# Optimization experiments

Hardware: AMD Instinct MI355X
Metric: run time of the kernel (lower is better)

The kernel has to match this reference:

```python
import jax, jax.numpy as jnp
import numpy as np

V, D, K, O, H = 20000, 256, 16, 128, 4
NEG_INF = -1e9


def setup_inputs() -> dict:
    key = jax.random.key(0)
    k1, k2, k3, k4 = jax.random.split(key, 4)
    x = jax.random.normal(k1, (V, D), dtype=jnp.float32)
    # padded adjacency list; value V (== mask_index) marks padding slots
    adj_lst = jax.random.randint(k2, (V, K), 0, V + 1, dtype=jnp.int64)
    W = jax.random.normal(k3, (H, D, O), dtype=jnp.float32) * 0.05  # per-head linear
    a = jax.random.normal(k4, (H, O), dtype=jnp.float32) * 0.05     # per-head attn vec
    b = jnp.zeros((H, O), dtype=jnp.float32)                         # per-head bias
    return {"x": x, "W": W, "a": a, "b": b, "adj_lst": adj_lst, "mask_index": V}


def reference(x, W, a, b, adj_lst, mask_index):
    # per-head linear transform: [H, V, O]
    t = jnp.einsum('vd,hdo->hvo', x, W)
    # per-node attention logits: [H, V]
    attn = jnp.einsum('hvo,ho->hv', t, a)
    pad = adj_lst == mask_index                      # [V, K] padding mask
    safe_idx = jnp.clip(adj_lst, 0, mask_index - 1)  # in-range gather indices
    # masked gather of neighbor attention logits: [H, V, K]
    scores = jnp.where(pad[None], NEG_INF, attn[:, safe_idx])
    coefs = jax.nn.softmax(scores, axis=-1)          # [H, V, K]
    # gather neighbor features and zero padded slots: [H, V, K, O]
    nbr = jnp.where(pad[None, :, :, None], 0.0, t[:, safe_idx])
    head = jnp.einsum('hvk,hvko->hvo', coefs, nbr) + b[:, None, :]
    out = jnp.mean(head, axis=0)                     # 1/H * add_n(heads)
    return jax.nn.relu(out)
```

## Files before the change

kernel.cpp:

```cpp
#include <hip/hip_runtime.h>


#define V_N 20000
#define D_N 256
#define K_N 16
#define O_N 128
#define H_N 4
#define NEG_INF -1e9f
#define TM 16

typedef _Float16 f16x8 __attribute__((ext_vector_type(8)));
typedef _Float16 f16x4 __attribute__((ext_vector_type(4)));
typedef float    f32x4 __attribute__((ext_vector_type(4)));

__global__ __launch_bounds__(256) void prep_kernel(
    const float* __restrict__ W, const float* __restrict__ a,
    _Float16* __restrict__ Wt, float* __restrict__ wt)
{
    if (blockIdx.x < 64) {
        const int idx  = blockIdx.x * 256 + threadIdx.x;
        const int lane = idx & 63;
        const int nt   = (idx >> 6) & 7;
        const int s    = (idx >> 9) & 7;
        const int h    = idx >> 12;
        const int o    = nt * 16 + (lane & 15);
        const int d0   = s * 32 + (lane >> 4) * 8;
        f16x8 v;
        #pragma unroll
        for (int j = 0; j < 8; ++j)
            v[j] = (_Float16)W[((size_t)h * D_N + d0 + j) * O_N + o];
        *(f16x8*)&Wt[(size_t)idx * 8] = v;
    } else {
        const int h = blockIdx.x - 64;
        const int d = threadIdx.x;
        const float* Wrow = W + ((size_t)h * D_N + d) * O_N;
        const float* ah   = a + h * O_N;
        float s = 0.f;
        #pragma unroll
        for (int o = 0; o < O_N; o += 4) {
            const float4 wv = *(const float4*)&Wrow[o];
            const float4 av = *(const float4*)&ah[o];
            s = fmaf(wv.x, av.x, s); s = fmaf(wv.y, av.y, s);
            s = fmaf(wv.z, av.z, s); s = fmaf(wv.w, av.w, s);
        }
        wt[h * D_N + d] = s;
    }
}

__global__ __launch_bounds__(256) void xsplit_attn_kernel(
    const float* __restrict__ x, const float* __restrict__ wt,
    _Float16* __restrict__ xh, float* __restrict__ attn4)
{
    const int wid  = threadIdx.x >> 6;
    const int lane = threadIdx.x & 63;
    const int v    = blockIdx.x * 4 + wid;

    const float4 p = *(const float4*)&x[(size_t)v * D_N + lane * 4];
    f16x4 hv = { (_Float16)p.x, (_Float16)p.y, (_Float16)p.z, (_Float16)p.w };
    *(f16x4*)&xh[(size_t)v * D_N + lane * 4] = hv;

    float s[H_N];
    #pragma unroll
    for (int h = 0; h < H_N; ++h) {
        const float4 w = *(const float4*)&wt[h * D_N + lane * 4];
        float t = fmaf(p.x, w.x, 0.f);
        t = fmaf(p.y, w.y, t); t = fmaf(p.z, w.z, t); t = fmaf(p.w, w.w, t);
        s[h] = t;
    }
    #pragma unroll
    for (int h = 0; h < H_N; ++h)
        #pragma unroll
        for (int dd = 32; dd >= 1; dd >>= 1)
            s[h] += __shfl_xor(s[h], dd);
    if (lane == 0)
        *(float4*)&attn4[(size_t)v * 4] = make_float4(s[0], s[1], s[2], s[3]);
}

__global__ __launch_bounds__(256, 4) void gat_kernel(
    const _Float16* __restrict__ xh, const float* __restrict__ attn4,
    const _Float16* __restrict__ Wt, const float* __restrict__ b,
    const int* __restrict__ adj, const int* __restrict__ mask_p,
    float* __restrict__ out)
{
    const int v0  = blockIdx.x * TM;
    const int tid = threadIdx.x;

    __shared__ int      sidx_s[TM][17];
    __shared__ float    coefs_s[K_N][17][H_N];
    __shared__ _Float16 yl[H_N * 512 * 8];

    {
        const int node = tid >> 4;
        const int k    = tid & 15;
        const int mask = mask_p[0];
        const int idx  = adj[(v0 + node) * K_N + k];
        const bool pad = (idx >= mask);
        const int safe = pad ? 0 : idx;
        const float4 av = *(const float4*)&attn4[(size_t)safe * 4];
        const float lg[H_N] = { pad ? NEG_INF : av.x, pad ? NEG_INF : av.y,
                                pad ? NEG_INF : av.z, pad ? NEG_INF : av.w };
        float c[H_N];
        #pragma unroll
        for (int h = 0; h < H_N; ++h) {
            float m = lg[h];
            #pragma unroll
            for (int s = 8; s >= 1; s >>= 1)
                m = fmaxf(m, __shfl_xor(m, s, 16));
            const float e = pad ? 0.f : __expf(lg[h] - m);
            float sum = e;
            #pragma unroll
            for (int s = 8; s >= 1; s >>= 1)
                sum += __shfl_xor(sum, s, 16);
            c[h] = pad ? 0.f : e / sum;
        }
        *(float4*)&coefs_s[k][node][0] = make_float4(c[0], c[1], c[2], c[3]);
        sidx_s[node][k] = safe;
    }
    __syncthreads();

    const int wid  = tid >> 6;
    const int lane = tid & 63;

    {
        const int hw = lane >> 5;
        const int sl = lane & 31;
        const _Float16* xsl = xh + sl * 8;

        float y[2][H_N][8];
        #pragma unroll
        for (int i = 0; i < 2; ++i)
            #pragma unroll
            for (int h = 0; h < H_N; ++h)
                #pragma unroll
                for (int j = 0; j < 8; ++j) y[i][h][j] = 0.f;

        #pragma unroll 4
        for (int k = 0; k < K_N; ++k) {
            #pragma unroll
            for (int i = 0; i < 2; ++i) {
                const int n  = wid * 4 + 2 * i + hw;
                const int si = sidx_s[n][k];
                const f16x8 xv = *(const f16x8*)&xsl[(size_t)si * D_N];
                const float4 c = *(const float4*)&coefs_s[k][n][0];
                const float ch4[H_N] = { c.x, c.y, c.z, c.w };
                #pragma unroll
                for (int h = 0; h < H_N; ++h)
                    #pragma unroll
                    for (int j = 0; j < 8; ++j)
                        y[i][h][j] = fmaf(ch4[h], (float)xv[j], y[i][h][j]);
            }
        }
        #pragma unroll
        for (int i = 0; i < 2; ++i) {
            const int n    = wid * 4 + 2 * i + hw;
            const int slot = n * 32 + (sl ^ n);
            #pragma unroll
            for (int h = 0; h < H_N; ++h) {
                f16x8 v;
                #pragma unroll
                for (int j = 0; j < 8; ++j) v[j] = (_Float16)y[i][h][j];
                *(f16x8*)&yl[(size_t)(h * 512 + slot) * 8] = v;
            }
        }
    }
    __syncthreads();

    const int m = lane & 15;
    const int q = lane >> 4;
    f32x4 acc0 = (f32x4){0.f, 0.f, 0.f, 0.f};
    f32x4 acc1 = (f32x4){0.f, 0.f, 0.f, 0.f};
    {
        const _Float16* Wb = Wt + (size_t)lane * 8;
        #pragma unroll
        for (int h = 0; h < H_N; ++h) {
            #pragma unroll
            for (int s = 0; s < 8; ++s) {
                const int slot = m * 32 + ((s * 4 + q) ^ m);
                const f16x8 af = *(const f16x8*)&yl[(size_t)(h * 512 + slot) * 8];
                const size_t fb = (size_t)((h * 8 + s) * 8 + wid * 2) * 512;
                const f16x8 b0 = *(const f16x8*)&Wb[fb];
                const f16x8 b1 = *(const f16x8*)&Wb[fb + 512];
                acc0 = __builtin_amdgcn_mfma_f32_16x16x32_f16(af, b0, acc0, 0, 0, 0);
                acc1 = __builtin_amdgcn_mfma_f32_16x16x32_f16(af, b1, acc1, 0, 0, 0);
            }
        }
    }

    #pragma unroll
    for (int nt = 0; nt < 2; ++nt) {
        const f32x4 acc = nt ? acc1 : acc0;
        const int col = (wid * 2 + nt) * 16 + m;
        const float bb = b[col] + b[O_N + col] + b[2 * O_N + col] + b[3 * O_N + col];
        #pragma unroll
        for (int r = 0; r < 4; ++r) {
            const int node = q * 4 + r;
            out[(size_t)(v0 + node) * O_N + col] = fmaxf(0.25f * (acc[r] + bb), 0.f);
        }
    }
}

extern "C" void kernel_launch(void* const* d_in, const int* in_sizes, int n_in,
                              void* d_out, int out_size, void* d_ws, size_t ws_size,
                              hipStream_t stream) {
    const float* x      = (const float*)d_in[0];
    const float* W      = (const float*)d_in[1];
    const float* a      = (const float*)d_in[2];
    const float* b      = (const float*)d_in[3];
    const int*   adj    = (const int*)d_in[4];
    const int*   mask_p = (const int*)d_in[5];
    float*       out    = (float*)d_out;

    char* p = (char*)d_ws;
    float*    attn4 = (float*)p;
    _Float16* xh    = (_Float16*)(p + 320000);
    _Float16* Wt    = (_Float16*)(p + 10560000);
    float*    wt    = (float*)(p + 10822144);

    prep_kernel<<<68, 256, 0, stream>>>(W, a, Wt, wt);
    xsplit_attn_kernel<<<V_N / 4, 256, 0, stream>>>(x, wt, xh, attn4);
    gat_kernel<<<V_N / TM, 256, 0, stream>>>(xh, attn4, Wt, b, adj, mask_p, out);
}
```

Before: 127.1 us.

## Split fused GAT kernel into separate aggregation and MFMA GEMM kernels

The single gather-plus-GEMM kernel becomes two kernels. An aggregation kernel with 512 threads gives each half-wave one node and writes the per-head aggregated fp16 features, already in MFMA fragment layout, to a global workspace. A second GEMM kernel then multiplies them by the pre-tiled W, with each wave computing a 16x64 output tile over all heads. This is meant to raise occupancy and parallelism in the gather phase and to give the GEMM better register reuse, at the cost of an extra global round trip (about 20 MB) and one more kernel launch.

```diff
diff --git a/kernel.cpp b/kernel.cpp
--- a/kernel.cpp
+++ b/kernel.cpp
@@ -7,7 +7,6 @@
 #define O_N 128
 #define H_N 4
 #define NEG_INF -1e9f
-#define TM 16
 
 typedef _Float16 f16x8 __attribute__((ext_vector_type(8)));
 typedef _Float16 f16x4 __attribute__((ext_vector_type(4)));
@@ -76,20 +75,19 @@
         *(float4*)&attn4[(size_t)v * 4] = make_float4(s[0], s[1], s[2], s[3]);
 }
 
-__global__ __launch_bounds__(256, 4) void gat_kernel(
+__global__ __launch_bounds__(512, 6) void agg_kernel(
     const _Float16* __restrict__ xh, const float* __restrict__ attn4,
-    const _Float16* __restrict__ Wt, const float* __restrict__ b,
     const int* __restrict__ adj, const int* __restrict__ mask_p,
-    float* __restrict__ out)
-{
-    const int v0  = blockIdx.x * TM;
+    _Float16* __restrict__ yg)
+{
+    const int v0  = blockIdx.x * 16;
     const int tid = threadIdx.x;
 
-    __shared__ int      sidx_s[TM][17];
+    __shared__ int      sidx_s[16][17];
     __shared__ float    coefs_s[K_N][17][H_N];
     __shared__ _Float16 yl[H_N * 512 * 8];
 
-    {
+    if (tid < 256) {
         const int node = tid >> 4;
         const int k    = tid & 15;
         const int mask = mask_p[0];
@@ -102,15 +100,15 @@
         float c[H_N];
         #pragma unroll
         for (int h = 0; h < H_N; ++h) {
-            float m = lg[h];
-            #pragma unroll
-            for (int s = 8; s >= 1; s >>= 1)
-                m = fmaxf(m, __shfl_xor(m, s, 16));
-            const float e = pad ? 0.f : __expf(lg[h] - m);
+            float mx = lg[h];
+            #pragma unroll
+            for (int s2 = 8; s2 >= 1; s2 >>= 1)
+                mx = fmaxf(mx, __shfl_xor(mx, s2, 16));
+            const float e = pad ? 0.f : __expf(lg[h] - mx);
             float sum = e;
             #pragma unroll
-            for (int s = 8; s >= 1; s >>= 1)
-                sum += __shfl_xor(sum, s, 16);
+            for (int s2 = 8; s2 >= 1; s2 >>= 1)
+                sum += __shfl_xor(sum, s2, 16);
             c[h] = pad ? 0.f : e / sum;
         }
         *(float4*)&coefs_s[k][node][0] = make_float4(c[0], c[1], c[2], c[3]);
@@ -118,83 +116,95 @@
     }
     __syncthreads();
 
-    const int wid  = tid >> 6;
+    const int w    = tid >> 6;
     const int lane = tid & 63;
+    const int hw   = lane >> 5;
+    const int sl   = lane & 31;
+    const int ln   = w * 2 + hw;
+
+    float y[H_N][8];
+    #pragma unroll
+    for (int h = 0; h < H_N; ++h)
+        #pragma unroll
+        for (int j = 0; j < 8; ++j) y[h][j] = 0.f;
+
+    const _Float16* xsl = xh + sl * 8;
+    #pragma unroll 2
+    for (int k = 0; k < K_N; ++k) {
+        const int si = sidx_s[ln][k];
+        const f16x8 xv = *(const f16x8*)&xsl[(size_t)si * D_N];
+        const float4 cc = *(const float4*)&coefs_s[k][ln][0];
+        const float ch4[H_N] = { cc.x, cc.y, cc.z, cc.w };
+        #pragma unroll
+        for (int h = 0; h < H_N; ++h)
+            #pragma unroll
+            for (int j = 0; j < 8; ++j)
+                y[h][j] = fmaf(ch4[h], (float)xv[j], y[h][j]);
+    }
 
     {
-        const int hw = lane >> 5;
-        const int sl = lane & 31;
-        const _Float16* xsl = xh + sl * 8;
-
-        float y[2][H_N][8];
-        #pragma unroll
-        for (int i = 0; i < 2; ++i)
-            #pragma unroll
-            for (int h = 0; h < H_N; ++h)
-                #pragma unroll
-                for (int j = 0; j < 8; ++j) y[i][h][j] = 0.f;
-
-        #pragma unroll 4
-        for (int k = 0; k < K_N; ++k) {
-            #pragma unroll
-            for (int i = 0; i < 2; ++i) {
-                const int n  = wid * 4 + 2 * i + hw;
-                const int si = sidx_s[n][k];
-                const f16x8 xv = *(const f16x8*)&xsl[(size_t)si * D_N];
-                const float4 c = *(const float4*)&coefs_s[k][n][0];
-                const float ch4[H_N] = { c.x, c.y, c.z, c.w };
-                #pragma unroll
-                for (int h = 0; h < H_N; ++h)
-                    #pragma unroll
-                    for (int j = 0; j < 8; ++j)
-                        y[i][h][j] = fmaf(ch4[h], (float)xv[j], y[i][h][j]);
-            }
-        }
-        #pragma unroll
-        for (int i = 0; i < 2; ++i) {
-            const int n    = wid * 4 + 2 * i + hw;
-            const int slot = n * 32 + (sl ^ n);
-            #pragma unroll
-            for (int h = 0; h < H_N; ++h) {
-                f16x8 v;
-                #pragma unroll
-                for (int j = 0; j < 8; ++j) v[j] = (_Float16)y[i][h][j];
-                *(f16x8*)&yl[(size_t)(h * 512 + slot) * 8] = v;
-            }
+        const int slot = ln * 32 + (sl ^ ln);
+        #pragma unroll
+        for (int h = 0; h < H_N; ++h) {
+            f16x8 v;
+            #pragma unroll
+            for (int j = 0; j < 8; ++j) v[j] = (_Float16)y[h][j];
+            *(f16x8*)&yl[(size_t)(h * 512 + slot) * 8] = v;
         }
     }
     __syncthreads();
 
-    const int m = lane & 15;
-    const int q = lane >> 4;
-    f32x4 acc0 = (f32x4){0.f, 0.f, 0.f, 0.f};
-    f32x4 acc1 = (f32x4){0.f, 0.f, 0.f, 0.f};
     {
-        const _Float16* Wb = Wt + (size_t)lane * 8;
+        const int s = tid >> 6;
+        const int m = lane & 15;
+        const int q = lane >> 4;
+        _Float16* ygb = yg + (size_t)blockIdx.x * (32 * 512);
         #pragma unroll
         for (int h = 0; h < H_N; ++h) {
-            #pragma unroll
-            for (int s = 0; s < 8; ++s) {
-                const int slot = m * 32 + ((s * 4 + q) ^ m);
-                const f16x8 af = *(const f16x8*)&yl[(size_t)(h * 512 + slot) * 8];
-                const size_t fb = (size_t)((h * 8 + s) * 8 + wid * 2) * 512;
-                const f16x8 b0 = *(const f16x8*)&Wb[fb];
-                const f16x8 b1 = *(const f16x8*)&Wb[fb + 512];
-                acc0 = __builtin_amdgcn_mfma_f32_16x16x32_f16(af, b0, acc0, 0, 0, 0);
-                acc1 = __builtin_amdgcn_mfma_f32_16x16x32_f16(af, b1, acc1, 0, 0, 0);
-            }
-        }
-    }
-
-    #pragma unroll
-    for (int nt = 0; nt < 2; ++nt) {
-        const f32x4 acc = nt ? acc1 : acc0;
-        const int col = (wid * 2 + nt) * 16 + m;
+            const int rs = m * 32 + ((((s << 2) | q)) ^ m);
+            const f16x8 v = *(const f16x8*)&yl[(size_t)(h * 512 + rs) * 8];
+            *(f16x8*)&ygb[((size_t)(h * 8 + s) * 64 + lane) * 8] = v;
+        }
+    }
+}
+
+__global__ __launch_bounds__(256, 6) void gemm_kernel(
+    const _Float16* __restrict__ yg, const _Float16* __restrict__ Wt,
+    const float* __restrict__ b, float* __restrict__ out)
+{
+    const int w    = threadIdx.x >> 6;
+    const int lane = threadIdx.x & 63;
+    const int mt   = blockIdx.x * 2 + (w >> 1);
+    const int nth  = (w & 1) * 4;
+
+    const _Float16* Ab = yg + (size_t)mt * (32 * 512) + lane * 8;
+    const _Float16* Bb = Wt + (size_t)nth * 512 + lane * 8;
+
+    f32x4 acc[4];
+    #pragma unroll
+    for (int nt = 0; nt < 4; ++nt) acc[nt] = (f32x4){0.f, 0.f, 0.f, 0.f};
+
+    #pragma unroll 2
+    for (int S = 0; S < 32; ++S) {
+        const f16x8 af = *(const f16x8*)&Ab[(size_t)S * 512];
+        #pragma unroll
+        for (int nt = 0; nt < 4; ++nt) {
+            const f16x8 bf = *(const f16x8*)&Bb[(size_t)(S * 8 + nt) * 512];
+            acc[nt] = __builtin_amdgcn_mfma_f32_16x16x32_f16(af, bf, acc[nt], 0, 0, 0);
+        }
+    }
+
+    const int m  = lane & 15;
+    const int q  = lane >> 4;
+    const int vb = mt * 16;
+    #pragma unroll
+    for (int nt = 0; nt < 4; ++nt) {
+        const int col = (nth + nt) * 16 + m;
         const float bb = b[col] + b[O_N + col] + b[2 * O_N + col] + b[3 * O_N + col];
         #pragma unroll
         for (int r = 0; r < 4; ++r) {
-            const int node = q * 4 + r;
-            out[(size_t)(v0 + node) * O_N + col] = fmaxf(0.25f * (acc[r] + bb), 0.f);
+            const int v = vb + q * 4 + r;
+            out[(size_t)v * O_N + col] = fmaxf(0.25f * (acc[nt][r] + bb), 0.f);
         }
     }
 }
@@ -215,8 +225,10 @@
     _Float16* xh    = (_Float16*)(p + 320000);
     _Float16* Wt    = (_Float16*)(p + 10560000);
     float*    wt    = (float*)(p + 10822144);
+    _Float16* yg    = (_Float16*)(p + 10826240);
 
     prep_kernel<<<68, 256, 0, stream>>>(W, a, Wt, wt);
     xsplit_attn_kernel<<<V_N / 4, 256, 0, stream>>>(x, wt, xh, attn4);
-    gat_kernel<<<V_N / TM, 256, 0, stream>>>(xh, attn4, Wt, b, adj, mask_p, out);
-}
+    agg_kernel<<<V_N / 16, 512, 0, stream>>>(xh, attn4, adj, mask_p, yg);
+    gemm_kernel<<<V_N / 32, 256, 0, stream>>>(yg, Wt, b, out);
+}
```

New measurement: 132.2 us. +4.0%, slower.

## Fuse three kernels into one persistent cooperative kernel with grid syncs

Applied to the files above, without the earlier changes.

Merges the weight-prep, x-conversion/attention-logit and GAT aggregation kernels into a single cooperative launch sized to the number of resident blocks. Grid-wide syncs separate the phases, and the later phases loop over nodes and tiles in a grid-stride fashion. This is meant to remove two kernel launch boundaries and their tail idle time. In exchange it pays for the grid.sync barriers, runs the small prep phase on a few blocks while the rest wait, and limits the gather phase to persistent blocks instead of 1250 independent ones.

```diff
diff --git a/kernel.cpp b/kernel.cpp
--- a/kernel.cpp
+++ b/kernel.cpp
@@ -1,4 +1,5 @@
 #include <hip/hip_runtime.h>
+#include <hip/hip_cooperative_groups.h>
 
 
 #define V_N 20000
@@ -13,26 +14,41 @@
 typedef _Float16 f16x4 __attribute__((ext_vector_type(4)));
 typedef float    f32x4 __attribute__((ext_vector_type(4)));
 
-__global__ __launch_bounds__(256) void prep_kernel(
-    const float* __restrict__ W, const float* __restrict__ a,
+namespace cg = cooperative_groups;
+
+__global__ __launch_bounds__(256, 4) void fused_kernel(
+    const float* __restrict__ x, const float* __restrict__ W,
+    const float* __restrict__ a, const float* __restrict__ b,
+    const int* __restrict__ adj, const int* __restrict__ mask_p,
+    float* __restrict__ out,
+    float* __restrict__ attn4, _Float16* __restrict__ xh,
     _Float16* __restrict__ Wt, float* __restrict__ wt)
 {
+    cg::grid_group grid = cg::this_grid();
+    const int tid  = threadIdx.x;
+    const int wid  = tid >> 6;
+    const int lane = tid & 63;
+
+    __shared__ int      sidx_s[TM][17];
+    __shared__ float    coefs_s[K_N][17][H_N];
+    __shared__ _Float16 yl[H_N * 512 * 8];
+
     if (blockIdx.x < 64) {
-        const int idx  = blockIdx.x * 256 + threadIdx.x;
-        const int lane = idx & 63;
-        const int nt   = (idx >> 6) & 7;
-        const int s    = (idx >> 9) & 7;
-        const int h    = idx >> 12;
-        const int o    = nt * 16 + (lane & 15);
-        const int d0   = s * 32 + (lane >> 4) * 8;
+        const int idx   = blockIdx.x * 256 + tid;
+        const int plane = idx & 63;
+        const int nt    = (idx >> 6) & 7;
+        const int s     = (idx >> 9) & 7;
+        const int h     = idx >> 12;
+        const int o     = nt * 16 + (plane & 15);
+        const int d0    = s * 32 + (plane >> 4) * 8;
         f16x8 v;
         #pragma unroll
         for (int j = 0; j < 8; ++j)
             v[j] = (_Float16)W[((size_t)h * D_N + d0 + j) * O_N + o];
         *(f16x8*)&Wt[(size_t)idx * 8] = v;
-    } else {
+    } else if (blockIdx.x < 68) {
         const int h = blockIdx.x - 64;
-        const int d = threadIdx.x;
+        const int d = tid;
         const float* Wrow = W + ((size_t)h * D_N + d) * O_N;
         const float* ah   = a + h * O_N;
         float s = 0.f;
@@ -45,156 +61,141 @@
         }
         wt[h * D_N + d] = s;
     }
-}
-
-__global__ __launch_bounds__(256) void xsplit_attn_kernel(
-    const float* __restrict__ x, const float* __restrict__ wt,
-    _Float16* __restrict__ xh, float* __restrict__ attn4)
-{
-    const int wid  = threadIdx.x >> 6;
-    const int lane = threadIdx.x & 63;
-    const int v    = blockIdx.x * 4 + wid;
-
-    const float4 p = *(const float4*)&x[(size_t)v * D_N + lane * 4];
-    f16x4 hv = { (_Float16)p.x, (_Float16)p.y, (_Float16)p.z, (_Float16)p.w };
-    *(f16x4*)&xh[(size_t)v * D_N + lane * 4] = hv;
-
-    float s[H_N];
-    #pragma unroll
-    for (int h = 0; h < H_N; ++h) {
-        const float4 w = *(const float4*)&wt[h * D_N + lane * 4];
-        float t = fmaf(p.x, w.x, 0.f);
-        t = fmaf(p.y, w.y, t); t = fmaf(p.z, w.z, t); t = fmaf(p.w, w.w, t);
-        s[h] = t;
-    }
-    #pragma unroll
-    for (int h = 0; h < H_N; ++h)
-        #pragma unroll
-        for (int dd = 32; dd >= 1; dd >>= 1)
-            s[h] += __shfl_xor(s[h], dd);
-    if (lane == 0)
-        *(float4*)&attn4[(size_t)v * 4] = make_float4(s[0], s[1], s[2], s[3]);
-}
-
-__global__ __launch_bounds__(256, 4) void gat_kernel(
-    const _Float16* __restrict__ xh, const float* __restrict__ attn4,
-    const _Float16* __restrict__ Wt, const float* __restrict__ b,
-    const int* __restrict__ adj, const int* __restrict__ mask_p,
-    float* __restrict__ out)
-{
-    const int v0  = blockIdx.x * TM;
-    const int tid = threadIdx.x;
-
-    __shared__ int      sidx_s[TM][17];
-    __shared__ float    coefs_s[K_N][17][H_N];
-    __shared__ _Float16 yl[H_N * 512 * 8];
+    grid.sync();
 
     {
-        const int node = tid >> 4;
-        const int k    = tid & 15;
-        const int mask = mask_p[0];
-        const int idx  = adj[(v0 + node) * K_N + k];
-        const bool pad = (idx >= mask);
-        const int safe = pad ? 0 : idx;
-        const float4 av = *(const float4*)&attn4[(size_t)safe * 4];
-        const float lg[H_N] = { pad ? NEG_INF : av.x, pad ? NEG_INF : av.y,
-                                pad ? NEG_INF : av.z, pad ? NEG_INF : av.w };
-        float c[H_N];
-        #pragma unroll
-        for (int h = 0; h < H_N; ++h) {
-            float m = lg[h];
-            #pragma unroll
-            for (int s = 8; s >= 1; s >>= 1)
-                m = fmaxf(m, __shfl_xor(m, s, 16));
-            const float e = pad ? 0.f : __expf(lg[h] - m);
-            float sum = e;
-            #pragma unroll
-            for (int s = 8; s >= 1; s >>= 1)
-                sum += __shfl_xor(sum, s, 16);
-            c[h] = pad ? 0.f : e / sum;
-        }
-        *(float4*)&coefs_s[k][node][0] = make_float4(c[0], c[1], c[2], c[3]);
-        sidx_s[node][k] = safe;
-    }
-    __syncthreads();
-
-    const int wid  = tid >> 6;
-    const int lane = tid & 63;
-
-    {
-        const int hw = lane >> 5;
-        const int sl = lane & 31;
-        const _Float16* xsl = xh + sl * 8;
-
-        float y[2][H_N][8];
-        #pragma unroll
-        for (int i = 0; i < 2; ++i)
+        const int nwave = gridDim.x * 4;
+        for (int v = blockIdx.x * 4 + wid; v < V_N; v += nwave) {
+            const float4 p = *(const float4*)&x[(size_t)v * D_N + lane * 4];
+            f16x4 hv = { (_Float16)p.x, (_Float16)p.y, (_Float16)p.z, (_Float16)p.w };
+            *(f16x4*)&xh[(size_t)v * D_N + lane * 4] = hv;
+
+            float s[H_N];
+            #pragma unroll
+            for (int h = 0; h < H_N; ++h) {
+                const float4 w = *(const float4*)&wt[h * D_N + lane * 4];
+                float t = fmaf(p.x, w.x, 0.f);
+                t = fmaf(p.y, w.y, t); t = fmaf(p.z, w.z, t); t = fmaf(p.w, w.w, t);
+                s[h] = t;
+            }
             #pragma unroll
             for (int h = 0; h < H_N; ++h)
                 #pragma unroll
-                for (int j = 0; j < 8; ++j) y[i][h][j] = 0.f;
-
-        #pragma unroll 4
-        for (int k = 0; k < K_N; ++k) {
-            #pragma unroll
-            for (int i = 0; i < 2; ++i) {
-                const int n  = wid * 4 + 2 * i + hw;
-                const int si = sidx_s[n][k];
-                const f16x8 xv = *(const f16x8*)&xsl[(size_t)si * D_N];
-                const float4 c = *(const float4*)&coefs_s[k][n][0];
-                const float ch4[H_N] = { c.x, c.y, c.z, c.w };
+                for (int dd = 32; dd >= 1; dd >>= 1)
+                    s[h] += __shfl_xor(s[h], dd);
+            if (lane == 0)
+                *(float4*)&attn4[(size_t)v * 4] = make_float4(s[0], s[1], s[2], s[3]);
+        }
+    }
+    grid.sync();
+
+    for (int t = blockIdx.x; t < V_N / TM; t += gridDim.x) {
+        const int v0 = t * TM;
+
+        {
+            const int node = tid >> 4;
+            const int k    = tid & 15;
+            const int mask = mask_p[0];
+            const int idx  = adj[(v0 + node) * K_N + k];
+            const bool pad = (idx >= mask);
+            const int safe = pad ? 0 : idx;
+            const float4 av = *(const float4*)&attn4[(size_t)safe * 4];
+            const float lg[H_N] = { pad ? NEG_INF : av.x, pad ? NEG_INF : av.y,
+                                    pad ? NEG_INF : av.z, pad ? NEG_INF : av.w };
+            float c[H_N];
+            #pragma unroll
+            for (int h = 0; h < H_N; ++h) {
+                float m = lg[h];
+                #pragma unroll
+                for (int s = 8; s >= 1; s >>= 1)
+                    m = fmaxf(m, __shfl_xor(m, s, 16));
+                const float e = pad ? 0.f : __expf(lg[h] - m);
+                float sum = e;
+                #pragma unroll
+                for (int s = 8; s >= 1; s >>= 1)
+                    sum += __shfl_xor(sum, s, 16);
+                c[h] = pad ? 0.f : e / sum;
+            }
+            *(float4*)&coefs_s[k][node][0] = make_float4(c[0], c[1], c[2], c[3]);
+            sidx_s[node][k] = safe;
+        }
+        __syncthreads();
+
+        {
+            const int hw = lane >> 5;
+            const int sl = lane & 31;
+            const _Float16* xsl = xh + sl * 8;
+
+            float y[2][H_N][8];
+            #pragma unroll
+            for (int i = 0; i < 2; ++i)
                 #pragma unroll
                 for (int h = 0; h < H_N; ++h)
                     #pragma unroll
-                    for (int j = 0; j < 8; ++j)
-                        y[i][h][j] = fmaf(ch4[h], (float)xv[j], y[i][h][j]);
-            }
-        }
+                    for (int j = 0; j < 8; ++j) y[i][h][j] = 0.f;
+
+            #pragma unroll 4
+            for (int k = 0; k < K_N; ++k) {
+                #pragma unroll
+                for (int i = 0; i < 2; ++i) {
+                    const int n  = wid * 4 + 2 * i + hw;
+                    const int si = sidx_s[n][k];
+                    const f16x8 xv = *(const f16x8*)&xsl[(size_t)si * D_N];
+                    const float4 c = *(const float4*)&coefs_s[k][n][0];
+                    const float ch4[H_N] = { c.x, c.y, c.z, c.w };
+                    #pragma unroll
+                    for (int h = 0; h < H_N; ++h)
+                        #pragma unroll
+                        for (int j = 0; j < 8; ++j)
+                            y[i][h][j] = fmaf(ch4[h], (float)xv[j], y[i][h][j]);
+                }
+            }
+            #pragma unroll
+            for (int i = 0; i < 2; ++i) {
+                const int n    = wid * 4 + 2 * i + hw;
+                const int slot = n * 32 + (sl ^ n);
+                #pragma unroll
+                for (int h = 0; h < H_N; ++h) {
+                    f16x8 v;
+                    #pragma unroll
+                    for (int j = 0; j < 8; ++j) v[j] = (_Float16)y[i][h][j];
+                    *(f16x8*)&yl[(size_t)(h * 512 + slot) * 8] = v;
+                }
+            }
+        }
+        __syncthreads();
+
+        const int m = lane & 15;
+        const int q = lane >> 4;
+        f32x4 acc0 = (f32x4){0.f, 0.f, 0.f, 0.f};
+        f32x4 acc1 = (f32x4){0.f, 0.f, 0.f, 0.f};
+        {
+            const _Float16* Wb = Wt + (size_t)lane * 8;
+            #pragma unroll
+            for (int h = 0; h < H_N; ++h) {
+                #pragma unroll
+                for (int s = 0; s < 8; ++s) {
+                    const int slot = m * 32 + ((s * 4 + q) ^ m);
+                    const f16x8 af = *(const f16x8*)&yl[(size_t)(h * 512 + slot) * 8];
+                    const size_t fb = (size_t)((h * 8 + s) * 8 + wid * 2) * 512;
+                    const f16x8 b0 = *(const f16x8*)&Wb[fb];
+                    const f16x8 b1 = *(const f16x8*)&Wb[fb + 512];
+                    acc0 = __builtin_amdgcn_mfma_f32_16x16x32_f16(af, b0, acc0, 0, 0, 0);
+                    acc1 = __builtin_amdgcn_mfma_f32_16x16x32_f16(af, b1, acc1, 0, 0, 0);
+                }
+            }
+        }
+
         #pragma unroll
-        for (int i = 0; i < 2; ++i) {
-            const int n    = wid * 4 + 2 * i + hw;
-            const int slot = n * 32 + (sl ^ n);
-            #pragma unroll
-            for (int h = 0; h < H_N; ++h) {
-                f16x8 v;
-                #pragma unroll
-                for (int j = 0; j < 8; ++j) v[j] = (_Float16)y[i][h][j];
-                *(f16x8*)&yl[(size_t)(h * 512 + slot) * 8] = v;
-            }
-        }
-    }
-    __syncthreads();
-
-    const int m = lane & 15;
-    const int q = lane >> 4;
-    f32x4 acc0 = (f32x4){0.f, 0.f, 0.f, 0.f};
-    f32x4 acc1 = (f32x4){0.f, 0.f, 0.f, 0.f};
-    {
-        const _Float16* Wb = Wt + (size_t)lane * 8;
-        #pragma unroll
-        for (int h = 0; h < H_N; ++h) {
-            #pragma unroll
-            for (int s = 0; s < 8; ++s) {
-                const int slot = m * 32 + ((s * 4 + q) ^ m);
-                const f16x8 af = *(const f16x8*)&yl[(size_t)(h * 512 + slot) * 8];
-                const size_t fb = (size_t)((h * 8 + s) * 8 + wid * 2) * 512;
-                const f16x8 b0 = *(const f16x8*)&Wb[fb];
-                const f16x8 b1 = *(const f16x8*)&Wb[fb + 512];
-                acc0 = __builtin_amdgcn_mfma_f32_16x16x32_f16(af, b0, acc0, 0, 0, 0);
-                acc1 = __builtin_amdgcn_mfma_f32_16x16x32_f16(af, b1, acc1, 0, 0, 0);
-            }
-        }
-    }
-
-    #pragma unroll
-    for (int nt = 0; nt < 2; ++nt) {
-        const f32x4 acc = nt ? acc1 : acc0;
-        const int col = (wid * 2 + nt) * 16 + m;
-        const float bb = b[col] + b[O_N + col] + b[2 * O_N + col] + b[3 * O_N + col];
-        #pragma unroll
-        for (int r = 0; r < 4; ++r) {
-            const int node = q * 4 + r;
-            out[(size_t)(v0 + node) * O_N + col] = fmaxf(0.25f * (acc[r] + bb), 0.f);
+        for (int nt = 0; nt < 2; ++nt) {
+            const f32x4 acc = nt ? acc1 : acc0;
+            const int col = (wid * 2 + nt) * 16 + m;
+            const float bb = b[col] + b[O_N + col] + b[2 * O_N + col] + b[3 * O_N + col];
+            #pragma unroll
+            for (int r = 0; r < 4; ++r) {
+                const int node = q * 4 + r;
+                out[(size_t)(v0 + node) * O_N + col] = fmaxf(0.25f * (acc[r] + bb), 0.f);
+            }
         }
     }
 }
@@ -216,7 +217,19 @@
     _Float16* Wt    = (_Float16*)(p + 10560000);
     float*    wt    = (float*)(p + 10822144);
 
-    prep_kernel<<<68, 256, 0, stream>>>(W, a, Wt, wt);
-    xsplit_attn_kernel<<<V_N / 4, 256, 0, stream>>>(x, wt, xh, attn4);
-    gat_kernel<<<V_N / TM, 256, 0, stream>>>(xh, attn4, Wt, b, adj, mask_p, out);
+    static int grid_blocks = 0;
+    if (grid_blocks == 0) {
+        int per_cu = 0, n_cu = 0;
+        hipOccupancyMaxActiveBlocksPerMultiprocessor(&per_cu, fused_kernel, 256, 0);
+        hipDeviceGetAttribute(&n_cu, hipDeviceAttributeMultiprocessorCount, 0);
+        if (per_cu < 1) per_cu = 4;
+        if (n_cu   < 1) n_cu   = 256;
+        grid_blocks = per_cu * n_cu;
+    }
+
+    void* args[] = { (void*)&x, (void*)&W, (void*)&a, (void*)&b,
+                     (void*)&adj, (void*)&mask_p, (void*)&out,
+                     (void*)&attn4, (void*)&xh, (void*)&Wt, (void*)&wt };
+    hipLaunchCooperativeKernel((const void*)fused_kernel,
+                               dim3(grid_blocks), dim3(256), args, 0, stream);
 }
```

New measurement: 324.8 us. +155.6%, slower.
